# Optimization experiments

Hardware: AMD Instinct MI355X
Metric: run time of the kernel (lower is better)

## Reference

```python
import jax, jax.numpy as jnp
import numpy as np


def setup_inputs() -> dict:
    key = jax.random.key(0)
    k1, k2, k3 = jax.random.split(key, 3)
    N, F, E, H = 50000, 256, 800000, 4
    P = F // H + 1            # proj = 65
    dk = P * H                # 260
    x = jax.random.normal(k1, (N, F), dtype=jnp.float32)
    W = jax.random.normal(k2, (2 * dk, F), dtype=jnp.float32) * 0.02
    b = jnp.zeros((2 * dk,), dtype=jnp.float32)
    edge_index = jax.random.randint(k3, (2, E), 0, N, dtype=jnp.int32)
    return {"x": x, "edge_index": edge_index, "W": W, "b": b, "num_heads": H}


def reference(x, edge_index, W, b, num_heads):
    # x: [N, F]; W: [2*dk, F] with dk = P*num_heads; edge_index: [2, E]
    N = x.shape[0]
    P = W.shape[0] // (2 * num_heads)
    qk = x @ W.T + b                                   # [N, 2*dk]
    qk = qk.reshape(N, num_heads, 2 * P)               # 'L (h hdim) -> L h hdim'
    q, k = qk[..., :P], qk[..., P:]                    # split=2 outer -> q then k, each [N, H, P]
    src, dst = edge_index[0], edge_index[1]
    # per-edge dot product per head (NB: original never applies self.scale)
    scores = jnp.einsum('ehp,ehp->eh', q[src], k[dst])  # [E, H]
    # sparse softmax over dim=2 (columns) i.e. segment-softmax grouped by row index per head
    smax = jax.ops.segment_max(scores, src, num_segments=N)  # [N, H]
    ex = jnp.exp(scores - smax[src])                         # [E, H]
    denom = jax.ops.segment_sum(ex, src, num_segments=N)     # [N, H]
    attn = ex / denom[src]                                   # [E, H]
    # torch.sparse.sum(attn, dim=0) / num_heads -> mean over heads per edge
    vals = attn.mean(axis=1)                                 # [E]
    return vals
```

## Files before the change

kernel.cpp:

```cpp
#include <hip/hip_runtime.h>
#include <hip/hip_bf16.h>

#define K_DIM 256
#define RQ    512
#define NPAD  640
#define GBM 128
#define GBN 128
#define GBK 32
#define EPITCH 152

typedef unsigned short u16;
using short8  = __attribute__((ext_vector_type(8))) short;
using ushort8 = __attribute__((ext_vector_type(8))) unsigned short;
using f32x4   = __attribute__((ext_vector_type(4))) float;
using f32x2   = __attribute__((ext_vector_type(2))) float;

__device__ __forceinline__ float asf(unsigned u) {
  union { unsigned i; float f; } x; x.i = u; return x.f;
}
__device__ __forceinline__ u16 f2b(float f) {
  __hip_bfloat16 h = __float2bfloat16(f); return *(u16*)&h;
}

__device__ __forceinline__ int map2(int p) {
  if (p < 256) return (p >> 6) * 130 + (p & 63);
  if (p < 512) { int q = p - 256; return (q >> 6) * 130 + 65 + (q & 63); }
  if (p < 516) return (p - 512) * 130 + 64;
  if (p < 520) return (p - 516) * 130 + 129;
  return -1;
}

__global__ void __launch_bounds__(256) prep(
    const float* __restrict__ x, const float* __restrict__ W,
    const float* __restrict__ bv,
    u16* __restrict__ xb, u16* __restrict__ wb,
    float* __restrict__ bias, float* __restrict__ denom,
    int M, int Mpad, int xblocks, int wblocks, int dn)
{
  const int blk = blockIdx.x, tid = threadIdx.x;
  if (blk < xblocks) {
    int idx = blk * 256 + tid;
    int total = Mpad * (K_DIM / 8);
    if (idx >= total) return;
    int row = idx / (K_DIM / 8);
    ushort8 o;
    if (row < M) {
      const float* s = x + (size_t)idx * 8;
      float4 a = *(const float4*)s;
      float4 b = *(const float4*)(s + 4);
      o[0] = f2b(a.x); o[1] = f2b(a.y); o[2] = f2b(a.z); o[3] = f2b(a.w);
      o[4] = f2b(b.x); o[5] = f2b(b.y); o[6] = f2b(b.z); o[7] = f2b(b.w);
    } else {
      #pragma unroll
      for (int j = 0; j < 8; ++j) o[j] = 0;
    }
    *(ushort8*)(xb + (size_t)idx * 8) = o;
  } else if (blk < xblocks + wblocks) {
    int idx = (blk - xblocks) * 256 + tid;
    int total = NPAD * (K_DIM / 8);
    if (idx >= total) return;
    int p  = idx / (K_DIM / 8);
    int kc = (idx % (K_DIM / 8)) * 8;
    int c  = map2(p);
    ushort8 o;
    if (c >= 0) {
      const float* s = W + (size_t)c * K_DIM + kc;
      float4 a = *(const float4*)s;
      float4 v = *(const float4*)(s + 4);
      o[0] = f2b(a.x); o[1] = f2b(a.y); o[2] = f2b(a.z); o[3] = f2b(a.w);
      o[4] = f2b(v.x); o[5] = f2b(v.y); o[6] = f2b(v.z); o[7] = f2b(v.w);
    } else {
      #pragma unroll
      for (int j = 0; j < 8; ++j) o[j] = 0;
    }
    *(ushort8*)(wb + (size_t)idx * 8) = o;
    if (kc == 0) bias[p] = (c >= 0) ? bv[c] : 0.f;
  } else {
    int i = (blk - xblocks - wblocks) * 256 + tid;
    if (i < dn) denom[i] = 0.f;
  }
}

__global__ void __launch_bounds__(256) gemm_mfma(
    const u16* __restrict__ xb, const u16* __restrict__ wb,
    const float* __restrict__ bias, u16* __restrict__ qkb,
    u16* __restrict__ tl, int M)
{
  __shared__ u16 smem[GBM * EPITCH];
  const int tid  = threadIdx.x;
  const int wave = tid >> 6, lane = tid & 63;
  const int l15 = lane & 15, lhi = lane >> 4;
  const int row0 = blockIdx.x * GBM, p0 = blockIdx.y * GBN;
  const int wr = (wave >> 1) * 64, wc = (wave & 1) * 64;

  f32x4 acc[4][4];
  #pragma unroll
  for (int m = 0; m < 4; ++m)
    #pragma unroll
    for (int n = 0; n < 4; ++n) acc[m][n] = (f32x4){0.f, 0.f, 0.f, 0.f};

#define STAGE(b, k0) do {                                                     \
    u16* As_ = smem + (b) * 8192;                                             \
    u16* Bs_ = As_ + 4096;                                                    \
    _Pragma("unroll")                                                         \
    for (int i_ = 0; i_ < 2; ++i_) {                                          \
      int f_ = wave * 128 + i_ * 64 + lane;                                   \
      int r_ = f_ >> 2, c_ = f_ & 3;                                          \
      const u16* gA = xb + (size_t)(row0 + r_) * K_DIM + (k0) + c_ * 8;       \
      __builtin_amdgcn_global_load_lds(                                       \
          (const __attribute__((address_space(1))) void*)gA,                  \
          (__attribute__((address_space(3))) void*)(As_ + (wave*128 + i_*64)*8), \
          16, 0, 0);                                                          \
      const u16* gB = wb + (size_t)(p0 + r_) * K_DIM + (k0) + c_ * 8;         \
      __builtin_amdgcn_global_load_lds(                                       \
          (const __attribute__((address_space(1))) void*)gB,                  \
          (__attribute__((address_space(3))) void*)(Bs_ + (wave*128 + i_*64)*8), \
          16, 0, 0);                                                          \
    }                                                                         \
  } while (0)

  STAGE(0, 0);
  asm volatile("s_waitcnt vmcnt(0)" ::: "memory");
  __syncthreads();

  #pragma unroll
  for (int t = 0; t < K_DIM / GBK; ++t) {
    if (t < K_DIM / GBK - 1) STAGE((t + 1) & 1, (t + 1) * GBK);
    const u16* As = smem + (t & 1) * 8192;
    const u16* Bs = As + 4096;
    short8 af[4], bf[4];
    #pragma unroll
    for (int m = 0; m < 4; ++m)
      af[m] = *(const short8*)(As + (size_t)(wr + m * 16 + l15) * GBK + lhi * 8);
    #pragma unroll
    for (int n = 0; n < 4; ++n)
      bf[n] = *(const short8*)(Bs + (size_t)(wc + n * 16 + l15) * GBK + lhi * 8);
    #pragma unroll
    for (int m = 0; m < 4; ++m)
      #pragma unroll
      for (int n = 0; n < 4; ++n)
        acc[m][n] = __builtin_amdgcn_mfma_f32_16x16x32_bf16(af[m], bf[n], acc[m][n], 0, 0, 0);
    if (t < K_DIM / GBK - 1) {
      asm volatile("s_waitcnt vmcnt(0)" ::: "memory");
      __syncthreads();
    }
  }
#undef STAGE

  __syncthreads();

  #pragma unroll
  for (int n = 0; n < 4; ++n) {
    int col = wc + n * 16 + l15;
    float bvv = bias[p0 + col];
    #pragma unroll
    for (int m = 0; m < 4; ++m) {
      #pragma unroll
      for (int r = 0; r < 4; ++r) {
        int row = wr + m * 16 + lhi * 4 + r;
        smem[row * EPITCH + col] = f2b(acc[m][n][r] + bvv);
      }
    }
  }
  __syncthreads();

  if (p0 < 512) {
    #pragma unroll
    for (int it = 0; it < 8; ++it) {
      int row  = wave * 32 + it * 4 + lhi;
      int grow = row0 + row;
      uint4 v = *(const uint4*)(smem + row * EPITCH + l15 * 8);
      if (grow < M)
        *(uint4*)(qkb + (size_t)grow * RQ + p0 + l15 * 8) = v;
    }
  } else {
    #pragma unroll
    for (int it = 0; it < 8; ++it) {
      int row  = wave * 32 + it * 4 + lhi;
      int grow = row0 + row;
      if (l15 == 0 && grow < M) {
        uint4 v = *(const uint4*)(smem + row * EPITCH);
        *(uint4*)(tl + (size_t)grow * 8) = v;
      }
    }
  }
}

__global__ void __launch_bounds__(256) edge_pass(
    const u16* __restrict__ qkb, const u16* __restrict__ tl,
    const int* __restrict__ ei,
    float* __restrict__ exb, float* __restrict__ denom, int E)
{
  const int tid  = threadIdx.x;
  const int wave = tid >> 6, lane = tid & 63;
  const int g = lane >> 3;
  const int l = lane & 7;
  const int e = (blockIdx.x * 4 + wave) * 8 + g;
  const bool valid = e < E;
  const int ec = valid ? e : 0;
  const int src = ei[ec];
  const int dst = ei[E + ec];

  const u16* qrow = qkb + ((size_t)src * RQ) + l * 32;
  const u16* krow = qkb + ((size_t)dst * RQ) + 256 + l * 32;

  int2 ti = make_int2(0, 0);
  if (l < 2) {
    const u16* tp = tl + (size_t)(l ? dst : src) * 8 + (l ? 4 : 0);
    ti = *(const int2*)tp;
  }

  f32x2 a2 = {0.f, 0.f};
  #pragma unroll
  for (int c = 0; c < 4; ++c) {
    uint4 qv = *(const uint4*)(qrow + c * 8);
    uint4 kv = *(const uint4*)(krow + c * 8);
    const unsigned* qd = (const unsigned*)&qv;
    const unsigned* kd = (const unsigned*)&kv;
    #pragma unroll
    for (int j = 0; j < 4; ++j) {
      f32x2 qa = { asf(qd[j] << 16), asf(qd[j] & 0xffff0000u) };
      f32x2 ka = { asf(kd[j] << 16), asf(kd[j] & 0xffff0000u) };
      a2 += qa * ka;
    }
  }
  float s = a2[0] + a2[1];
  s += __shfl_xor(s, 1);

  const int h = l >> 1;
  int idxA = ((g << 3) | (l & 1)) << 2;
  int w01 = __builtin_amdgcn_ds_bpermute(idxA, ti.x);
  int w23 = __builtin_amdgcn_ds_bpermute(idxA, ti.y);
  unsigned wsel = (h & 2) ? (unsigned)w23 : (unsigned)w01;
  float tv = (h & 1) ? asf(wsel & 0xffff0000u) : asf(wsel << 16);
  float to = __shfl_xor(tv, 1);
  s = fmaf(tv, to, s);

  float ev = __expf(s);
  if (valid && (l & 1) == 0) {
    exb[(size_t)e * 4 + h] = ev;
    unsafeAtomicAdd(&denom[(size_t)src * 4 + h], ev);
  }
}

__global__ void __launch_bounds__(256) finalize_k(
    const float* __restrict__ exb, const float* __restrict__ denom,
    const int* __restrict__ ei, float* __restrict__ out, int E)
{
  int e = blockIdx.x * 256 + threadIdx.x;
  if (e >= E) return;
  int src = ei[e];
  float4 ev = *(const float4*)(exb + (size_t)e * 4);
  float4 dv = *(const float4*)(denom + (size_t)src * 4);
  out[e] = 0.25f * (ev.x / dv.x + ev.y / dv.y + ev.z / dv.z + ev.w / dv.w);
}

extern "C" void kernel_launch(void* const* d_in, const int* in_sizes, int n_in,
                              void* d_out, int out_size, void* d_ws, size_t ws_size,
                              hipStream_t stream)
{
  const float* x  = (const float*)d_in[0];
  const int*   ei = (const int*)d_in[1];
  const float* W  = (const float*)d_in[2];
  const float* b  = (const float*)d_in[3];

  const int F = in_sizes[2] / in_sizes[3];
  const int M = in_sizes[0] / F;
  const int E = in_sizes[1] / 2;

  const int mblocks = (M + GBM - 1) / GBM;
  const int Mpad    = mblocks * GBM;

  u16* xb  = (u16*)d_ws;
  u16* wb  = xb + (size_t)Mpad * K_DIM;
  u16* qkb = wb + (size_t)NPAD * K_DIM;
  u16* tl  = qkb + (size_t)M * RQ;
  float* bias  = (float*)(tl + (size_t)M * 8);
  float* exb   = bias + NPAD;
  float* denom = exb + (size_t)E * 4;

  const int xblocks = (Mpad * (K_DIM / 8) + 255) / 256;
  const int wblocks = (NPAD * (K_DIM / 8) + 255) / 256;
  const int dn      = M * 4;
  const int zblocks = (dn + 255) / 256;
  hipLaunchKernelGGL(prep, dim3(xblocks + wblocks + zblocks), dim3(256), 0, stream,
                     x, W, b, xb, wb, bias, denom, M, Mpad, xblocks, wblocks, dn);

  dim3 gg(mblocks, NPAD / GBN);
  hipLaunchKernelGGL(gemm_mfma, gg, dim3(256), 0, stream, xb, wb, bias, qkb, tl, M);

  int eblocks = (E + 31) / 32;
  hipLaunchKernelGGL(edge_pass, dim3(eblocks), dim3(256), 0, stream,
                     qkb, tl, ei, exb, denom, E);

  hipLaunchKernelGGL(finalize_k, dim3((E + 255) / 256), dim3(256), 0, stream,
                     exb, denom, ei, (float*)d_out, E);
}
```

Before: 180.9 us.

## Bucket edges by source block and swizzle edge blocks across XCDs

Adds a histogram, scan and scatter pass that counting-sorts edges into buckets of 64 source nodes. The edge pass then reads (src, dst, edge id) triples in bucketed order, with a block-index swizzle so that neighbouring buckets land on the same XCD. The aim is better L2 reuse of q rows and more local atomics on denom. In exchange it adds three kernels, a 16-byte-per-edge scatter with atomic cursors, and a single-block scan that depends on NB ≤ 1024.

```diff
diff --git a/kernel.cpp b/kernel.cpp
--- a/kernel.cpp
+++ b/kernel.cpp
@@ -8,6 +8,7 @@
 #define GBN 128
 #define GBK 32
 #define EPITCH 152
+#define NBP   800
 
 typedef unsigned short u16;
 using short8  = __attribute__((ext_vector_type(8))) short;
@@ -34,8 +35,8 @@
     const float* __restrict__ x, const float* __restrict__ W,
     const float* __restrict__ bv,
     u16* __restrict__ xb, u16* __restrict__ wb,
-    float* __restrict__ bias, float* __restrict__ denom,
-    int M, int Mpad, int xblocks, int wblocks, int dn)
+    float* __restrict__ bias, float* __restrict__ zbase,
+    int M, int Mpad, int xblocks, int wblocks, int zn)
 {
   const int blk = blockIdx.x, tid = threadIdx.x;
   if (blk < xblocks) {
@@ -77,7 +78,7 @@
     if (kc == 0) bias[p] = (c >= 0) ? bv[c] : 0.f;
   } else {
     int i = (blk - xblocks - wblocks) * 256 + tid;
-    if (i < dn) denom[i] = 0.f;
+    if (i < zn) zbase[i] = 0.f;
   }
 }
 
@@ -186,20 +187,62 @@
   }
 }
 
+__global__ void __launch_bounds__(256) hist_k(
+    const int* __restrict__ ei, int* __restrict__ cnt, int E)
+{
+  int i = blockIdx.x * 256 + threadIdx.x;
+  if (i < E) atomicAdd(&cnt[ei[i] >> 6], 1);
+}
+
+__global__ void __launch_bounds__(1024) scan_k(
+    const int* __restrict__ cnt, int* __restrict__ cursor, int NB)
+{
+  __shared__ int s[1024];
+  int t = threadIdx.x;
+  int own = (t < NB) ? cnt[t] : 0;
+  s[t] = own;
+  __syncthreads();
+  #pragma unroll
+  for (int off = 1; off < 1024; off <<= 1) {
+    int u = (t >= off) ? s[t - off] : 0;
+    __syncthreads();
+    s[t] += u;
+    __syncthreads();
+  }
+  if (t < NB) cursor[t] = s[t] - own;
+}
+
+__global__ void __launch_bounds__(256) scatter_k(
+    const int* __restrict__ ei, int* __restrict__ cursor,
+    uint4* __restrict__ sorted, int E)
+{
+  int i = blockIdx.x * 256 + threadIdx.x;
+  if (i >= E) return;
+  int src = ei[i], dst = ei[E + i];
+  int pos = atomicAdd(&cursor[src >> 6], 1);
+  sorted[pos] = make_uint4((unsigned)src, (unsigned)dst, (unsigned)i, 0u);
+}
+
 __global__ void __launch_bounds__(256) edge_pass(
     const u16* __restrict__ qkb, const u16* __restrict__ tl,
-    const int* __restrict__ ei,
+    const uint4* __restrict__ sorted,
     float* __restrict__ exb, float* __restrict__ denom, int E)
 {
   const int tid  = threadIdx.x;
   const int wave = tid >> 6, lane = tid & 63;
   const int g = lane >> 3;
   const int l = lane & 7;
-  const int e = (blockIdx.x * 4 + wave) * 8 + g;
-  const bool valid = e < E;
-  const int ec = valid ? e : 0;
-  const int src = ei[ec];
-  const int dst = ei[E + ec];
+
+  const int nwg = gridDim.x;
+  const int q8 = nwg >> 3, r8 = nwg & 7;
+  const int xcd = blockIdx.x & 7, bix = blockIdx.x >> 3;
+  const int swz = (xcd < r8) ? (xcd * (q8 + 1) + bix)
+                             : (r8 * (q8 + 1) + (xcd - r8) * q8 + bix);
+
+  const int slot = swz * 32 + wave * 8 + g;
+  const bool valid = slot < E;
+  uint4 tr = sorted[valid ? slot : 0];
+  const int src = tr.x, dst = tr.y, e = tr.z;
 
   const u16* qrow = qkb + ((size_t)src * RQ) + l * 32;
   const u16* krow = qkb + ((size_t)dst * RQ) + 256 + l * 32;
@@ -267,6 +310,7 @@
   const int F = in_sizes[2] / in_sizes[3];
   const int M = in_sizes[0] / F;
   const int E = in_sizes[1] / 2;
+  const int NB = (M + 63) >> 6;
 
   const int mblocks = (M + GBM - 1) / GBM;
   const int Mpad    = mblocks * GBM;
@@ -278,20 +322,29 @@
   float* bias  = (float*)(tl + (size_t)M * 8);
   float* exb   = bias + NPAD;
   float* denom = exb + (size_t)E * 4;
+  int*   cnt    = (int*)(denom + (size_t)M * 4);
+  int*   cursor = cnt + NBP;
+  uint4* sorted = (uint4*)(cursor + NBP);
 
   const int xblocks = (Mpad * (K_DIM / 8) + 255) / 256;
   const int wblocks = (NPAD * (K_DIM / 8) + 255) / 256;
-  const int dn      = M * 4;
-  const int zblocks = (dn + 255) / 256;
+  const int zn      = M * 4 + 2 * NBP;
+  const int zblocks = (zn + 255) / 256;
   hipLaunchKernelGGL(prep, dim3(xblocks + wblocks + zblocks), dim3(256), 0, stream,
-                     x, W, b, xb, wb, bias, denom, M, Mpad, xblocks, wblocks, dn);
+                     x, W, b, xb, wb, bias, denom, M, Mpad, xblocks, wblocks, zn);
+
+  const int eb256 = (E + 255) / 256;
+  hipLaunchKernelGGL(hist_k, dim3(eb256), dim3(256), 0, stream, ei, cnt, E);
+  hipLaunchKernelGGL(scan_k, dim3(1), dim3(1024), 0, stream, cnt, cursor, NB);
 
   dim3 gg(mblocks, NPAD / GBN);
   hipLaunchKernelGGL(gemm_mfma, gg, dim3(256), 0, stream, xb, wb, bias, qkb, tl, M);
 
+  hipLaunchKernelGGL(scatter_k, dim3(eb256), dim3(256), 0, stream, ei, cursor, sorted, E);
+
   int eblocks = (E + 31) / 32;
   hipLaunchKernelGGL(edge_pass, dim3(eblocks), dim3(256), 0, stream,
-                     qkb, tl, ei, exb, denom, E);
+                     qkb, tl, sorted, exb, denom, E);
 
   hipLaunchKernelGGL(finalize_k, dim3((E + 255) / 256), dim3(256), 0, stream,
                      exb, denom, ei, (float*)d_out, E);
```

New measurement: 545.7 us. +201.6%, slower.
